# Kernel tuning notes

Measured on AMD Instinct MI355X. Metric: run time of the kernel, lower is better.

Reference implementation:

```python
import jax, jax.numpy as jnp
import numpy as np

H = 512
W = 512
NSH = 4
MU_BORDER = 1.05
S_MIN = 1.0 / 30.0   # 1 / n_gaussian_max_pixels
S_MAX = 1.0 / 0.75   # 1 / n_gaussian_min_pixels
B = 8192
N = 2048


def setup_inputs() -> dict:
    key = jax.random.key(0)
    k1, k2, k3, k4, k5, k6 = jax.random.split(key, 6)
    x_bx2 = jax.random.uniform(k1, (B, 2), dtype=jnp.float32) * jnp.array([W, H], jnp.float32)
    xyz = jax.random.uniform(k2, (N, 2), dtype=jnp.float32) * 2.0 - 1.0
    features = jax.random.uniform(k3, (N, 2 * NSH + 1, 3), dtype=jnp.float32)
    opacity = 0.1 + 0.9 * jax.random.uniform(k4, (N,), dtype=jnp.float32)
    scaling = jax.random.uniform(k5, (N, 2), dtype=jnp.float32)
    rotation = jax.random.uniform(k6, (N,), dtype=jnp.float32)
    return dict(x_bx2=x_bx2, xyz=xyz, features=features, opacity=opacity,
                scaling=scaling, rotation=rotation)


def reference(x_bx2, xyz, features, opacity, scaling, rotation):
    wh = jnp.array([W, H], x_bx2.dtype)
    xnorm = x_bx2 / wh * 2.0 - 1.0                      # [b,2] in [-1,1]
    mu = jnp.clip(xyz, -1.0, 1.0) * MU_BORDER           # [n,2]
    S = jnp.clip(scaling, 0.0, 1.0) * (S_MAX - S_MIN) + S_MIN   # [n,2]
    ang = jnp.remainder(rotation, 1.0) * (2.0 * jnp.pi)  # [n]
    c = jnp.cos(ang)
    s = jnp.sin(ang)

    # pixel-space offset point - mu: [b,n,2]
    vec = (xnorm[:, None, :] - mu[None, :, :]) * 0.5 * wh
    vx = vec[..., 0]
    vy = vec[..., 1]
    # rotated: R @ v with R = [[c,-s],[s,c]]
    rx = c * vx - s * vy
    ry = s * vx + c * vy
    # scaled Mahalanobis-style squared distance
    d2 = (S[:, 0] * rx) ** 2 + (S[:, 1] * ry) ** 2       # [b,n]
    # validity test done in torch under no_grad: ||S*R*v|| < 5
    valid = jax.lax.stop_gradient(d2) < 25.0

    # unit direction point->gaussian, rotated, then angle for SH basis
    vn = jnp.sqrt(vx * vx + vy * vy)
    inv = 1.0 / (1e-10 + vn)
    nx = vx * inv
    ny = vy * inv
    rnx = c * nx - s * ny
    rny = s * nx + c * ny
    theta = jnp.arctan2(rnx, rny)                        # [b,n] (atan2(rot_x, rot_y) as in torch)

    # SH basis: [1, sin(th), cos(th), sin(2th), cos(2th), ...] -> [b,n,2*NSH+1]
    ks = jnp.arange(1, NSH + 1, dtype=theta.dtype)
    tk = theta[..., None] * ks                           # [b,n,NSH]
    sc = jnp.stack([jnp.sin(tk), jnp.cos(tk)], axis=-1).reshape(*theta.shape, 2 * NSH)
    basis = jnp.concatenate([jnp.ones_like(theta)[..., None], sc], axis=-1)

    rgb = jax.nn.sigmoid(jnp.einsum('bnm,nmc->bnc', basis, features))  # [b,n,3]
    wgt = jnp.exp(-d2) * jnp.clip(opacity, 0.0, 1.0) * valid.astype(rgb.dtype)  # [b,n]
    # accumulate_along_rays == per-ray weighted sum of rgb
    return jnp.einsum('bn,bnc->bc', wgt, rgb)            # [b,3]
```

## Files before the change

### kernel.cpp

```cpp
#include <hip/hip_runtime.h>


constexpr int   BN    = 8192;
constexpr int   NG    = 2048;
constexpr float SMIN  = 1.0f / 30.0f;
constexpr float SSPAN = (1.0f / 0.75f - 1.0f / 30.0f);
constexpr float MUSCALE = 1.05f * 256.0f;
constexpr float LOG2E = 1.44269504088896341f;
constexpr float QT    = 25.0f * 1.44269504088896341f;
constexpr float TWOPI = 6.283185307179586f;
constexpr int   BLOCK = 256;
constexpr int   RC    = 4;
constexpr int   NBLK  = BN / RC;
constexpr int   GPT   = NG / BLOCK;
constexpr int   QMAX  = 2048;

__global__ __launch_bounds__(BLOCK) void splat_one(
    const float* __restrict__ xb,
    const float* __restrict__ xyz,
    const float* __restrict__ feat,
    const float* __restrict__ opac,
    const float* __restrict__ scal,
    const float* __restrict__ rot,
    float* __restrict__ out)
{
    __shared__ float    sray[RC * 2];
    __shared__ float    sacc[RC * 3];
    __shared__ unsigned queue[QMAX];
    __shared__ int      qcnt;

    const int tid = threadIdx.x;
    const int rc  = blockIdx.x;

    if (tid == 0) qcnt = 0;
    if (tid < RC) {
        const float2 t = reinterpret_cast<const float2*>(xb)[rc * RC + tid];
        sray[2 * tid + 0] = t.x - 256.0f;
        sray[2 * tid + 1] = t.y - 256.0f;
    }
    if (tid < RC * 3) sacc[tid] = 0.0f;
    __syncthreads();

    float rxs[RC], rys[RC];
    #pragma unroll
    for (int i = 0; i < RC; ++i) { rxs[i] = sray[2 * i]; rys[i] = sray[2 * i + 1]; }

    float2 xy = reinterpret_cast<const float2*>(xyz)[tid];
    float2 sc = reinterpret_cast<const float2*>(scal)[tid];
    float  rr = rot[tid];

    for (int k = 0; k < GPT; ++k) {
        float2 nxy, nsc; float nrr;
        if (k + 1 < GPT) {
            const int gn = (k + 1) * BLOCK + tid;
            nxy = reinterpret_cast<const float2*>(xyz)[gn];
            nsc = reinterpret_cast<const float2*>(scal)[gn];
            nrr = rot[gn];
        }
        const float mx = fminf(fmaxf(xy.x, -1.0f), 1.0f) * MUSCALE;
        const float my = fminf(fmaxf(xy.y, -1.0f), 1.0f) * MUSCALE;
        const float s0 = fminf(fmaxf(sc.x, 0.0f), 1.0f) * SSPAN + SMIN;
        const float s1 = fminf(fmaxf(sc.y, 0.0f), 1.0f) * SSPAN + SMIN;
        const float ang = (rr - floorf(rr)) * TWOPI;
        float sn, cs;
        __sincosf(ang, &sn, &cs);
        const float qsx = s0 * s0 * LOG2E;
        const float qsy = s1 * s1 * LOG2E;
        const float c2 = cs * cs, s2 = sn * sn;
        const float A  = fmaf(qsx, c2, qsy * s2);
        const float C  = fmaf(qsx, s2, qsy * c2);
        const float Bq = 2.0f * cs * sn * (qsy - qsx);
        const unsigned gbase = (unsigned)(k * BLOCK + tid) << 2;

        #pragma unroll
        for (int i = 0; i < RC; ++i) {
            const float vx = rxs[i] - mx;
            const float vy = rys[i] - my;
            const float q  = fmaf(A, vx * vx, fmaf(Bq, vx * vy, C * (vy * vy)));
            if (q < QT) {
                const int idx = atomicAdd(&qcnt, 1);
                if (idx < QMAX) queue[idx] = gbase | (unsigned)i;
            }
        }
        xy = nxy; sc = nsc; rr = nrr;
    }
    __syncthreads();

    const int n = min(qcnt, QMAX);
    for (int j = tid; j < n; j += BLOCK) {
        const unsigned e = queue[j];
        const int g = (int)(e >> 2);
        const int i = (int)(e & 3u);

        const float2 gxy = reinterpret_cast<const float2*>(xyz)[g];
        const float2 gsc = reinterpret_cast<const float2*>(scal)[g];
        const float  grr = rot[g];
        const float  op  = fminf(fmaxf(opac[g], 0.0f), 1.0f);
        const float mx = fminf(fmaxf(gxy.x, -1.0f), 1.0f) * MUSCALE;
        const float my = fminf(fmaxf(gxy.y, -1.0f), 1.0f) * MUSCALE;
        const float s0 = fminf(fmaxf(gsc.x, 0.0f), 1.0f) * SSPAN + SMIN;
        const float s1 = fminf(fmaxf(gsc.y, 0.0f), 1.0f) * SSPAN + SMIN;
        const float ang = (grr - floorf(grr)) * TWOPI;
        float sn, cs;
        __sincosf(ang, &sn, &cs);

        const float vx = sray[2 * i + 0] - mx;
        const float vy = sray[2 * i + 1] - my;
        const float rx = fmaf(cs, vx, -sn * vy);
        const float ry = fmaf(sn, vx,  cs * vy);
        const float q  = fmaf(s0 * s0 * LOG2E, rx * rx,
                              (s1 * s1 * LOG2E) * (ry * ry));
        const float w  = exp2f(log2f(fmaxf(op, 1e-30f)) - q);

        const float iv  = rsqrtf(fmaxf(vx * vx + vy * vy, 1e-24f));
        const float s1v = rx * iv;
        const float c1v = ry * iv;
        const float s2v = 2.0f * s1v * c1v;
        const float c2v = fmaf(-2.0f * s1v, s1v, 1.0f);
        const float s3v = fmaf(s1v, c2v, c1v * s2v);
        const float c3v = fmaf(c1v, c2v, -s1v * s2v);
        const float s4v = 2.0f * s2v * c2v;
        const float c4v = fmaf(-2.0f * s2v, s2v, 1.0f);

        const float* __restrict__ fg = feat + (size_t)g * 27;
        float x0 = fg[0], x1 = fg[1], x2 = fg[2];
        x0 = fmaf(s1v, fg[3],  x0); x1 = fmaf(s1v, fg[4],  x1); x2 = fmaf(s1v, fg[5],  x2);
        x0 = fmaf(c1v, fg[6],  x0); x1 = fmaf(c1v, fg[7],  x1); x2 = fmaf(c1v, fg[8],  x2);
        x0 = fmaf(s2v, fg[9],  x0); x1 = fmaf(s2v, fg[10], x1); x2 = fmaf(s2v, fg[11], x2);
        x0 = fmaf(c2v, fg[12], x0); x1 = fmaf(c2v, fg[13], x1); x2 = fmaf(c2v, fg[14], x2);
        x0 = fmaf(s3v, fg[15], x0); x1 = fmaf(s3v, fg[16], x1); x2 = fmaf(s3v, fg[17], x2);
        x0 = fmaf(c3v, fg[18], x0); x1 = fmaf(c3v, fg[19], x1); x2 = fmaf(c3v, fg[20], x2);
        x0 = fmaf(s4v, fg[21], x0); x1 = fmaf(s4v, fg[22], x1); x2 = fmaf(s4v, fg[23], x2);
        x0 = fmaf(c4v, fg[24], x0); x1 = fmaf(c4v, fg[25], x1); x2 = fmaf(c4v, fg[26], x2);

        atomicAdd(&sacc[3 * i + 0], __fdividef(w, 1.0f + exp2f(-x0 * LOG2E)));
        atomicAdd(&sacc[3 * i + 1], __fdividef(w, 1.0f + exp2f(-x1 * LOG2E)));
        atomicAdd(&sacc[3 * i + 2], __fdividef(w, 1.0f + exp2f(-x2 * LOG2E)));
    }
    __syncthreads();

    if (tid < RC * 3)
        out[rc * (RC * 3) + tid] = sacc[tid];
}

extern "C" void kernel_launch(void* const* d_in, const int* in_sizes, int n_in,
                              void* d_out, int out_size, void* d_ws, size_t ws_size,
                              hipStream_t stream) {
    const float* xb   = (const float*)d_in[0];
    const float* xyz  = (const float*)d_in[1];
    const float* feat = (const float*)d_in[2];
    const float* opac = (const float*)d_in[3];
    const float* scal = (const float*)d_in[4];
    const float* rot  = (const float*)d_in[5];
    float* out = (float*)d_out;

    splat_one<<<dim3(NBLK), dim3(BLOCK), 0, stream>>>(
        xb, xyz, feat, opac, scal, rot, out);
}
```

Measured before the change: 15.82 us.

## Precompute per-Gaussian quadratic params in a prepass and double rays per block

Adds a small prepass kernel that computes each Gaussian's clamped mean, quadratic-form coefficients, log2 opacity and rotation cos/sin once, and stores them as two float4s in workspace. The main kernel reads these instead of recomputing the clamps, sincos and coefficients in every block and for every queued hit. Rays per block go from 4 to 8, which halves the block count and spreads the per-Gaussian loads over more rays. The cost is an extra kernel launch and a global-memory round trip, plus a larger queue load per block with the same QMAX of 2048, so overflow becomes more likely.

```diff
diff --git a/kernel.cpp b/kernel.cpp
--- a/kernel.cpp
+++ b/kernel.cpp
@@ -10,18 +10,45 @@
 constexpr float QT    = 25.0f * 1.44269504088896341f;
 constexpr float TWOPI = 6.283185307179586f;
 constexpr int   BLOCK = 256;
-constexpr int   RC    = 4;
+constexpr int   RC    = 8;
 constexpr int   NBLK  = BN / RC;
 constexpr int   GPT   = NG / BLOCK;
 constexpr int   QMAX  = 2048;
 
-__global__ __launch_bounds__(BLOCK) void splat_one(
+__global__ __launch_bounds__(256) void splat_pre(
+    const float* __restrict__ xyz, const float* __restrict__ opac,
+    const float* __restrict__ scal, const float* __restrict__ rot,
+    float* __restrict__ gp)
+{
+    const int g = blockIdx.x * 256 + threadIdx.x;
+    if (g >= NG) return;
+    const float2 xy = reinterpret_cast<const float2*>(xyz)[g];
+    const float2 sc = reinterpret_cast<const float2*>(scal)[g];
+    const float  rr = rot[g];
+    const float  op = fminf(fmaxf(opac[g], 0.0f), 1.0f);
+    const float mx = fminf(fmaxf(xy.x, -1.0f), 1.0f) * MUSCALE;
+    const float my = fminf(fmaxf(xy.y, -1.0f), 1.0f) * MUSCALE;
+    const float s0 = fminf(fmaxf(sc.x, 0.0f), 1.0f) * SSPAN + SMIN;
+    const float s1 = fminf(fmaxf(sc.y, 0.0f), 1.0f) * SSPAN + SMIN;
+    const float ang = (rr - floorf(rr)) * TWOPI;
+    const float cs = cosf(ang);
+    const float sn = sinf(ang);
+    const float qsx = s0 * s0 * LOG2E;
+    const float qsy = s1 * s1 * LOG2E;
+    const float c2 = cs * cs, s2 = sn * sn;
+    const float A  = fmaf(qsx, c2, qsy * s2);
+    const float C  = fmaf(qsx, s2, qsy * c2);
+    const float Bq = 2.0f * cs * sn * (qsy - qsx);
+    const float l2op = log2f(fmaxf(op, 1e-30f));
+    float4* o = reinterpret_cast<float4*>(gp + 8 * g);
+    o[0] = make_float4(mx, my, A, Bq);
+    o[1] = make_float4(C, l2op, cs, sn);
+}
+
+__global__ __launch_bounds__(BLOCK) void splat_main(
     const float* __restrict__ xb,
-    const float* __restrict__ xyz,
+    const float* __restrict__ gp,
     const float* __restrict__ feat,
-    const float* __restrict__ opac,
-    const float* __restrict__ scal,
-    const float* __restrict__ rot,
     float* __restrict__ out)
 {
     __shared__ float    sray[RC * 2];
@@ -45,33 +72,15 @@
     #pragma unroll
     for (int i = 0; i < RC; ++i) { rxs[i] = sray[2 * i]; rys[i] = sray[2 * i + 1]; }
 
-    float2 xy = reinterpret_cast<const float2*>(xyz)[tid];
-    float2 sc = reinterpret_cast<const float2*>(scal)[tid];
-    float  rr = rot[tid];
+    const float4* __restrict__ gp4 = reinterpret_cast<const float4*>(gp);
 
+    float4 p0 = gp4[2 * tid + 0];
     for (int k = 0; k < GPT; ++k) {
-        float2 nxy, nsc; float nrr;
-        if (k + 1 < GPT) {
-            const int gn = (k + 1) * BLOCK + tid;
-            nxy = reinterpret_cast<const float2*>(xyz)[gn];
-            nsc = reinterpret_cast<const float2*>(scal)[gn];
-            nrr = rot[gn];
-        }
-        const float mx = fminf(fmaxf(xy.x, -1.0f), 1.0f) * MUSCALE;
-        const float my = fminf(fmaxf(xy.y, -1.0f), 1.0f) * MUSCALE;
-        const float s0 = fminf(fmaxf(sc.x, 0.0f), 1.0f) * SSPAN + SMIN;
-        const float s1 = fminf(fmaxf(sc.y, 0.0f), 1.0f) * SSPAN + SMIN;
-        const float ang = (rr - floorf(rr)) * TWOPI;
-        float sn, cs;
-        __sincosf(ang, &sn, &cs);
-        const float qsx = s0 * s0 * LOG2E;
-        const float qsy = s1 * s1 * LOG2E;
-        const float c2 = cs * cs, s2 = sn * sn;
-        const float A  = fmaf(qsx, c2, qsy * s2);
-        const float C  = fmaf(qsx, s2, qsy * c2);
-        const float Bq = 2.0f * cs * sn * (qsy - qsx);
-        const unsigned gbase = (unsigned)(k * BLOCK + tid) << 2;
-
+        float4 n0;
+        if (k + 1 < GPT) n0 = gp4[2 * ((k + 1) * BLOCK + tid)];
+        const float mx = p0.x, my = p0.y, A = p0.z, Bq = p0.w;
+        const float C  = gp4[2 * (k * BLOCK + tid) + 1].x;
+        const unsigned gbase = (unsigned)(k * BLOCK + tid) << 3;
         #pragma unroll
         for (int i = 0; i < RC; ++i) {
             const float vx = rxs[i] - mx;
@@ -82,35 +91,25 @@
                 if (idx < QMAX) queue[idx] = gbase | (unsigned)i;
             }
         }
-        xy = nxy; sc = nsc; rr = nrr;
+        p0 = n0;
     }
     __syncthreads();
 
     const int n = min(qcnt, QMAX);
     for (int j = tid; j < n; j += BLOCK) {
         const unsigned e = queue[j];
-        const int g = (int)(e >> 2);
-        const int i = (int)(e & 3u);
+        const int g = (int)(e >> 3);
+        const int i = (int)(e & 7u);
 
-        const float2 gxy = reinterpret_cast<const float2*>(xyz)[g];
-        const float2 gsc = reinterpret_cast<const float2*>(scal)[g];
-        const float  grr = rot[g];
-        const float  op  = fminf(fmaxf(opac[g], 0.0f), 1.0f);
-        const float mx = fminf(fmaxf(gxy.x, -1.0f), 1.0f) * MUSCALE;
-        const float my = fminf(fmaxf(gxy.y, -1.0f), 1.0f) * MUSCALE;
-        const float s0 = fminf(fmaxf(gsc.x, 0.0f), 1.0f) * SSPAN + SMIN;
-        const float s1 = fminf(fmaxf(gsc.y, 0.0f), 1.0f) * SSPAN + SMIN;
-        const float ang = (grr - floorf(grr)) * TWOPI;
-        float sn, cs;
-        __sincosf(ang, &sn, &cs);
-
-        const float vx = sray[2 * i + 0] - mx;
-        const float vy = sray[2 * i + 1] - my;
+        const float4 a = gp4[2 * g + 0];
+        const float4 b = gp4[2 * g + 1];
+        const float vx = sray[2 * i + 0] - a.x;
+        const float vy = sray[2 * i + 1] - a.y;
+        const float q  = fmaf(a.z, vx * vx, fmaf(a.w, vx * vy, b.x * (vy * vy)));
+        const float w  = exp2f(b.y - q);
+        const float cs = b.z, sn = b.w;
         const float rx = fmaf(cs, vx, -sn * vy);
         const float ry = fmaf(sn, vx,  cs * vy);
-        const float q  = fmaf(s0 * s0 * LOG2E, rx * rx,
-                              (s1 * s1 * LOG2E) * (ry * ry));
-        const float w  = exp2f(log2f(fmaxf(op, 1e-30f)) - q);
 
         const float iv  = rsqrtf(fmaxf(vx * vx + vy * vy, 1e-24f));
         const float s1v = rx * iv;
@@ -153,7 +152,8 @@
     const float* scal = (const float*)d_in[4];
     const float* rot  = (const float*)d_in[5];
     float* out = (float*)d_out;
+    float* gp  = (float*)d_ws;
 
-    splat_one<<<dim3(NBLK), dim3(BLOCK), 0, stream>>>(
-        xb, xyz, feat, opac, scal, rot, out);
+    splat_pre<<<dim3(NG / 256), dim3(256), 0, stream>>>(xyz, opac, scal, rot, gp);
+    splat_main<<<dim3(NBLK), dim3(BLOCK), 0, stream>>>(xb, gp, feat, out);
 }
```

New measurement: 18.10 us. 1.14x slower.

## Process eight rays per block and stage culling parameters as packed fp16

Applied to the files above, without the earlier changes.

Each block now handles eight rays instead of four, so each per-Gaussian conic setup (clamps, sincos, quadratic coefficients) is shared across more rays and the grid has half as many blocks. The setup is done in a separate first pass and stored as packed half2 values in shared memory. The culling pass then reads those values back and unpacks them to float. The fp16 rounding of centres and coefficients can flip the validity test for borderline ray/Gaussian pairs. The extra 24 KB of shared memory may lower occupancy, and the exact phase now uses the slower precise cosf/sinf.

```diff
diff --git a/kernel.cpp b/kernel.cpp
--- a/kernel.cpp
+++ b/kernel.cpp
@@ -1,4 +1,5 @@
 #include <hip/hip_runtime.h>
+#include <hip/hip_fp16.h>
 
 
 constexpr int   BN    = 8192;
@@ -10,10 +11,19 @@
 constexpr float QT    = 25.0f * 1.44269504088896341f;
 constexpr float TWOPI = 6.283185307179586f;
 constexpr int   BLOCK = 256;
-constexpr int   RC    = 4;
+constexpr int   RC    = 8;
 constexpr int   NBLK  = BN / RC;
 constexpr int   GPT   = NG / BLOCK;
 constexpr int   QMAX  = 2048;
+
+static __device__ __forceinline__ unsigned pk2h(float a, float b) {
+    __half2 h = __floats2half2_rn(a, b);
+    return __builtin_bit_cast(unsigned, h);
+}
+static __device__ __forceinline__ float2 unpk(unsigned u) {
+    __half2 h = __builtin_bit_cast(__half2, u);
+    return __half22float2(h);
+}
 
 __global__ __launch_bounds__(BLOCK) void splat_one(
     const float* __restrict__ xb,
@@ -24,6 +34,7 @@
     const float* __restrict__ rot,
     float* __restrict__ out)
 {
+    __shared__ unsigned su0[NG], su1[NG], su2[NG];
     __shared__ float    sray[RC * 2];
     __shared__ float    sacc[RC * 3];
     __shared__ unsigned queue[QMAX];
@@ -39,24 +50,13 @@
         sray[2 * tid + 1] = t.y - 256.0f;
     }
     if (tid < RC * 3) sacc[tid] = 0.0f;
-    __syncthreads();
 
-    float rxs[RC], rys[RC];
     #pragma unroll
-    for (int i = 0; i < RC; ++i) { rxs[i] = sray[2 * i]; rys[i] = sray[2 * i + 1]; }
-
-    float2 xy = reinterpret_cast<const float2*>(xyz)[tid];
-    float2 sc = reinterpret_cast<const float2*>(scal)[tid];
-    float  rr = rot[tid];
-
     for (int k = 0; k < GPT; ++k) {
-        float2 nxy, nsc; float nrr;
-        if (k + 1 < GPT) {
-            const int gn = (k + 1) * BLOCK + tid;
-            nxy = reinterpret_cast<const float2*>(xyz)[gn];
-            nsc = reinterpret_cast<const float2*>(scal)[gn];
-            nrr = rot[gn];
-        }
+        const int g = k * BLOCK + tid;
+        const float2 xy = reinterpret_cast<const float2*>(xyz)[g];
+        const float2 sc = reinterpret_cast<const float2*>(scal)[g];
+        const float  rr = rot[g];
         const float mx = fminf(fmaxf(xy.x, -1.0f), 1.0f) * MUSCALE;
         const float my = fminf(fmaxf(xy.y, -1.0f), 1.0f) * MUSCALE;
         const float s0 = fminf(fmaxf(sc.x, 0.0f), 1.0f) * SSPAN + SMIN;
@@ -70,39 +70,53 @@
         const float A  = fmaf(qsx, c2, qsy * s2);
         const float C  = fmaf(qsx, s2, qsy * c2);
         const float Bq = 2.0f * cs * sn * (qsy - qsx);
-        const unsigned gbase = (unsigned)(k * BLOCK + tid) << 2;
+        su0[g] = pk2h(mx, my);
+        su1[g] = pk2h(A, Bq);
+        su2[g] = pk2h(C, 0.0f);
+    }
+    __syncthreads();
 
+    float rxs[RC], rys[RC];
+    #pragma unroll
+    for (int i = 0; i < RC; ++i) { rxs[i] = sray[2 * i]; rys[i] = sray[2 * i + 1]; }
+
+    #pragma unroll
+    for (int k = 0; k < GPT; ++k) {
+        const int g = k * BLOCK + tid;
+        const float2 m  = unpk(su0[g]);
+        const float2 ab = unpk(su1[g]);
+        const float2 cc = unpk(su2[g]);
         #pragma unroll
         for (int i = 0; i < RC; ++i) {
-            const float vx = rxs[i] - mx;
-            const float vy = rys[i] - my;
-            const float q  = fmaf(A, vx * vx, fmaf(Bq, vx * vy, C * (vy * vy)));
+            const float vx = rxs[i] - m.x;
+            const float vy = rys[i] - m.y;
+            const float q  = fmaf(ab.x, vx * vx,
+                             fmaf(ab.y, vx * vy, cc.x * (vy * vy)));
             if (q < QT) {
                 const int idx = atomicAdd(&qcnt, 1);
-                if (idx < QMAX) queue[idx] = gbase | (unsigned)i;
+                if (idx < QMAX) queue[idx] = ((unsigned)g << 3) | (unsigned)i;
             }
         }
-        xy = nxy; sc = nsc; rr = nrr;
     }
     __syncthreads();
 
     const int n = min(qcnt, QMAX);
     for (int j = tid; j < n; j += BLOCK) {
         const unsigned e = queue[j];
-        const int g = (int)(e >> 2);
-        const int i = (int)(e & 3u);
+        const int g = (int)(e >> 3);
+        const int i = (int)(e & 7u);
 
-        const float2 gxy = reinterpret_cast<const float2*>(xyz)[g];
-        const float2 gsc = reinterpret_cast<const float2*>(scal)[g];
-        const float  grr = rot[g];
-        const float  op  = fminf(fmaxf(opac[g], 0.0f), 1.0f);
-        const float mx = fminf(fmaxf(gxy.x, -1.0f), 1.0f) * MUSCALE;
-        const float my = fminf(fmaxf(gxy.y, -1.0f), 1.0f) * MUSCALE;
-        const float s0 = fminf(fmaxf(gsc.x, 0.0f), 1.0f) * SSPAN + SMIN;
-        const float s1 = fminf(fmaxf(gsc.y, 0.0f), 1.0f) * SSPAN + SMIN;
-        const float ang = (grr - floorf(grr)) * TWOPI;
-        float sn, cs;
-        __sincosf(ang, &sn, &cs);
+        const float2 xy = reinterpret_cast<const float2*>(xyz)[g];
+        const float2 sc = reinterpret_cast<const float2*>(scal)[g];
+        const float  rr = rot[g];
+        const float  op = fminf(fmaxf(opac[g], 0.0f), 1.0f);
+        const float mx = fminf(fmaxf(xy.x, -1.0f), 1.0f) * MUSCALE;
+        const float my = fminf(fmaxf(xy.y, -1.0f), 1.0f) * MUSCALE;
+        const float s0 = fminf(fmaxf(sc.x, 0.0f), 1.0f) * SSPAN + SMIN;
+        const float s1 = fminf(fmaxf(sc.y, 0.0f), 1.0f) * SSPAN + SMIN;
+        const float ang = (rr - floorf(rr)) * TWOPI;
+        const float cs = cosf(ang);
+        const float sn = sinf(ang);
 
         const float vx = sray[2 * i + 0] - mx;
         const float vy = sray[2 * i + 1] - my;
```

New measurement: 15.24 us. -3.7%, faster.
